# Kernel tuning notes

Measured on AMD Instinct MI355X. Metric: run time of the kernel, lower is better.

Reference implementation:

```python
import jax, jax.numpy as jnp
import numpy as np

B, T, D_MODEL = 1, 2048, 4096
NUM_Q_HEADS, NUM_KV_HEADS, KEY_SIZE = 32, 8, 128
ATTN_MULT = 0.08838834764831845  # 1/sqrt(key_size)
MAX_ATTN_VAL = 30.0


def rotate_half(x):
    x1, x2 = jnp.split(x, 2, axis=-1)
    return jnp.concatenate((-x2, x1), axis=-1)


def apply_rope(x):
    # x: [b, t, h, d]; offset = 0, positions = arange(t)
    b, t, h, d = x.shape
    exponents = jnp.arange(0, d, 2, dtype=jnp.float32)
    inv_freq = 1.0 / (10000.0 ** (exponents / d))            # [d/2]
    pos = jnp.arange(t, dtype=jnp.float32)                   # [t]
    phase = pos[:, None] * inv_freq[None, :]                 # [t, d/2]
    phase = jnp.tile(phase, (1, 2))[None, :, None, :]        # [1, t, 1, d] (tiled, not interleaved)
    return (x * jnp.cos(phase) + rotate_half(x) * jnp.sin(phase)).astype(x.dtype)


def setup_inputs() -> dict:
    key = jax.random.key(0)
    ks = jax.random.split(key, 8)
    query = jax.random.normal(ks[0], (B, T, D_MODEL), dtype=jnp.float32)
    kk = jax.random.normal(ks[1], (B, T, D_MODEL), dtype=jnp.float32)
    vv = jax.random.normal(ks[2], (B, T, D_MODEL), dtype=jnp.float32)
    mask = jnp.tril(jnp.ones((T, T), dtype=bool))[None, None, :, :]  # causal [1,1,T,T]
    s = 0.02
    Wq = jax.random.normal(ks[3], (D_MODEL, NUM_Q_HEADS * KEY_SIZE), dtype=jnp.float32) * s
    Wk = jax.random.normal(ks[4], (D_MODEL, NUM_KV_HEADS * KEY_SIZE), dtype=jnp.float32) * s
    Wv = jax.random.normal(ks[5], (D_MODEL, NUM_KV_HEADS * KEY_SIZE), dtype=jnp.float32) * s
    Wo = jax.random.normal(ks[6], (NUM_Q_HEADS * KEY_SIZE, D_MODEL), dtype=jnp.float32) * s
    return {"query": query, "key": kk, "value": vv, "mask": mask,
            "Wq": Wq, "Wk": Wk, "Wv": Wv, "Wo": Wo}


def reference(query, key, value, mask, Wq, Wk, Wv, Wo):
    b, t, _ = query.shape
    d = KEY_SIZE
    h, kv_h = NUM_Q_HEADS, NUM_KV_HEADS
    g = h // kv_h
    # projections (no bias)
    q = (query @ Wq).reshape(b, t, h, d)
    k = (key @ Wk).reshape(b, t, kv_h, d)
    v = (value @ Wv).reshape(b, t, kv_h, d)
    # RoPE on q and k
    q = apply_rope(q)
    k = apply_rope(k)
    # GQA grouping: [b, t, kv_h, g, d]
    q = q.reshape(b, t, kv_h, g, d)
    logits = jnp.einsum('btkgd,bTkd->bkgtT', q, k).astype(jnp.float32)
    logits = logits * ATTN_MULT
    logits = MAX_ATTN_VAL * jnp.tanh(logits / MAX_ATTN_VAL)  # soft-capping
    m = mask[:, :, None, :, :]  # [b,1,1,t,T]
    logits = jnp.where(m, logits, -1e30)
    weights = jax.nn.softmax(logits, axis=-1).astype(query.dtype)
    attn = jnp.einsum('bkgtT,bTkd->btkgd', weights, v)
    attn = attn.reshape(b, t, h * d)
    return attn @ Wo
```

## Files before the change

kernel.cpp:

```cpp
#include <hip/hip_runtime.h>
#include <hip/hip_bf16.h>
#include <stdint.h>
#include <stddef.h>

#define T_SEQ 2048
#define DM    4096
#define NQH   32
#define NKVH  8
#define HD    128
#define ATTN_MULT 0.08838834764831845f

typedef __attribute__((ext_vector_type(8))) short bf16x8;
typedef __attribute__((ext_vector_type(4))) float f32x4;
typedef __attribute__((ext_vector_type(4))) unsigned int u32x4;

__device__ __forceinline__ unsigned short f2b(float f) {
  unsigned u = __builtin_bit_cast(unsigned, f);
  u = u + 0x7FFFu + ((u >> 16) & 1u);
  return (unsigned short)(u >> 16);
}
__device__ __forceinline__ float b2f(unsigned short h) {
  unsigned u = ((unsigned)h) << 16;
  return __builtin_bit_cast(float, u);
}
__device__ __forceinline__ unsigned cvt_pk_bf16(float lo, float hi) {
  unsigned r;
  asm("v_cvt_pk_bf16_f32 %0, %1, %2" : "=v"(r) : "v"(lo), "v"(hi));
  return r;
}

typedef const __attribute__((address_space(1))) void* gptr1_t;
typedef __attribute__((address_space(3))) void* lptr3_t;
__device__ __forceinline__ void gl_lds16(const void* g, void* l) {
  __builtin_amdgcn_global_load_lds((gptr1_t)g, (lptr3_t)l, 16, 0, 0);
}

#define MFMA16(a, b, c) __builtin_amdgcn_mfma_f32_16x16x32_bf16((a), (b), (c), 0, 0, 0)

__global__ __launch_bounds__(256) void transpose_cast4_kernel(
    const float* __restrict__ Wq, const float* __restrict__ Wk,
    const float* __restrict__ Wv, const float* __restrict__ Wo,
    unsigned short* __restrict__ WqT, unsigned short* __restrict__ WkT,
    unsigned short* __restrict__ WvT, unsigned short* __restrict__ WoT) {
  __shared__ float tile[64][65];
  int y = blockIdx.y;
  const float* W;
  unsigned short* WT;
  int N, n0;
  if (y < 64)      { W = Wq; WT = WqT; N = 4096; n0 = y * 64; }
  else if (y < 80) { W = Wk; WT = WkT; N = 1024; n0 = (y - 64) * 64; }
  else if (y < 96) { W = Wv; WT = WvT; N = 1024; n0 = (y - 80) * 64; }
  else             { W = Wo; WT = WoT; N = 4096; n0 = (y - 96) * 64; }
  const int K = 4096;
  int k0 = blockIdx.x * 64;
  int t = threadIdx.x;
  int rr = t >> 4;
  int cc = t & 15;
#pragma unroll
  for (int c = 0; c < 4; ++c) {
    int row = c * 16 + rr;
    float4 v = *(const float4*)&W[(size_t)(k0 + row) * N + n0 + cc * 4];
    tile[row][cc * 4 + 0] = v.x;
    tile[row][cc * 4 + 1] = v.y;
    tile[row][cc * 4 + 2] = v.z;
    tile[row][cc * 4 + 3] = v.w;
  }
  __syncthreads();
  int orow = t >> 2;
  int kb = (t & 3) * 16;
  u32x4 o1, o2;
#pragma unroll
  for (int u = 0; u < 4; ++u) {
    o1[u] = (unsigned)f2b(tile[kb + 2 * u][orow]) |
            ((unsigned)f2b(tile[kb + 2 * u + 1][orow]) << 16);
    o2[u] = (unsigned)f2b(tile[kb + 8 + 2 * u][orow]) |
            ((unsigned)f2b(tile[kb + 9 + 2 * u][orow]) << 16);
  }
  unsigned short* dst = &WT[(size_t)(n0 + orow) * K + k0 + kb];
  *(u32x4*)dst = o1;
  *(u32x4*)(dst + 8) = o2;
}

__global__ __launch_bounds__(256) void cast3_kernel(
    const float* __restrict__ a0, const float* __restrict__ a1, const float* __restrict__ a2,
    unsigned short* __restrict__ b0, unsigned short* __restrict__ b1, unsigned short* __restrict__ b2) {
  const float* in = blockIdx.z == 0 ? a0 : (blockIdx.z == 1 ? a1 : a2);
  unsigned short* out = blockIdx.z == 0 ? b0 : (blockIdx.z == 1 ? b1 : b2);
  size_t idx = ((size_t)blockIdx.x * 256 + threadIdx.x) * 8;
  float4 x = *(const float4*)(in + idx);
  float4 y = *(const float4*)(in + idx + 4);
  u32x4 v;
  v[0] = (unsigned)f2b(x.x) | ((unsigned)f2b(x.y) << 16);
  v[1] = (unsigned)f2b(x.z) | ((unsigned)f2b(x.w) << 16);
  v[2] = (unsigned)f2b(y.x) | ((unsigned)f2b(y.y) << 16);
  v[3] = (unsigned)f2b(y.z) | ((unsigned)f2b(y.w) << 16);
  *(u32x4*)(out + idx) = v;
}

template <bool F32OUT>
__device__ __forceinline__ void gemm256_body(
    unsigned short* lds,
    const unsigned short* __restrict__ A, const unsigned short* __restrict__ BT,
    void* __restrict__ C, int N, int Klen, int Kstride, int m0, int n0) {
  int t = threadIdx.x;
  int w = t >> 6, l = t & 63;
  int wm = w >> 2, wn = w & 3;
  int lr = l & 15, lh = l >> 4;

  f32x4 acc[8][4] = {};

  int scb = (((l & 7) ^ (l >> 3)) & 7) << 4;
  const int NT = Klen >> 6;
  int rswz = (lr & 7) << 4;
  int cb0 = (lh * 16) ^ rswz;
  int cb1 = (64 + lh * 16) ^ rswz;

  auto stageT = [&](const unsigned short* X, int base, int tt, int c, int ldsoff) {
#pragma unroll
    for (int h = 0; h < 2; ++h) {
      int grow = base + h * 128 + w * 8 + (l >> 3);
      const char* s1 = (const char*)X + ((size_t)grow * Kstride + tt * 64) * 2 + scb;
      gl_lds16(s1, (char*)lds + c * 65536 + ldsoff + h * 16384 + w * 1024);
      const char* s2 = (const char*)X + ((size_t)(grow + 64) * Kstride + tt * 64) * 2 + scb;
      gl_lds16(s2, (char*)lds + c * 65536 + ldsoff + h * 16384 + 8192 + w * 1024);
    }
  };

  stageT(A, m0, 0, 0, 0);
  stageT(BT, n0, 0, 0, 32768);
  asm volatile("s_waitcnt vmcnt(0)" ::: "memory");
  __builtin_amdgcn_s_barrier();

  for (int tt = 0; tt < NT; ++tt) {
    const char* Ab = (const char*)lds + (tt & 1) * 65536;
    const char* Bb = Ab + 32768;
    if (tt + 1 < NT) {
      int nb = (tt + 1) & 1;
      stageT(A, m0, tt + 1, nb, 0);
      stageT(BT, n0, tt + 1, nb, 32768);
    }
    int arow = wm * 128 + lr;
    int brow = wn * 64 + lr;
#pragma unroll
    for (int ks = 0; ks < 2; ++ks) {
      int cb = ks ? cb1 : cb0;
      bf16x8 av[8], bv[4];
#pragma unroll
      for (int i = 0; i < 8; ++i)
        av[i] = *(const bf16x8*)(Ab + (arow + i * 16) * 128 + cb);
#pragma unroll
      for (int j = 0; j < 4; ++j)
        bv[j] = *(const bf16x8*)(Bb + (brow + j * 16) * 128 + cb);
#pragma unroll
      for (int i = 0; i < 8; ++i)
#pragma unroll
        for (int j = 0; j < 4; ++j)
          acc[i][j] = MFMA16(av[i], bv[j], acc[i][j]);
    }
    asm volatile("s_waitcnt vmcnt(0)" ::: "memory");
    __builtin_amdgcn_s_barrier();
  }

#pragma unroll
  for (int i = 0; i < 8; ++i) {
#pragma unroll
    for (int j = 0; j < 4; ++j) {
#pragma unroll
      for (int r = 0; r < 4; ++r) {
        int row = m0 + wm * 128 + i * 16 + lh * 4 + r;
        int col = n0 + wn * 64 + j * 16 + lr;
        if constexpr (F32OUT)
          ((float*)C)[(size_t)row * N + col] = acc[i][j][r];
        else
          ((unsigned short*)C)[(size_t)row * N + col] = f2b(acc[i][j][r]);
      }
    }
  }
}

__global__ __launch_bounds__(512, 1) void qkv256_kernel(
    const unsigned short* __restrict__ qb, const unsigned short* __restrict__ WqT, unsigned short* __restrict__ Qp,
    const unsigned short* __restrict__ kb, const unsigned short* __restrict__ WkT, unsigned short* __restrict__ Kp,
    const unsigned short* __restrict__ vb, const unsigned short* __restrict__ WvT, unsigned short* __restrict__ Vp) {
  __shared__ unsigned short lds[2 * 32768];
  int flat = blockIdx.x;
  const unsigned short *A, *BT;
  unsigned short* C;
  int N, m0, n0;
  if (flat < 128) {
    A = qb; BT = WqT; C = Qp; N = NQH * HD;
    m0 = (flat >> 4) * 256;
    n0 = (flat & 15) * 256;
  } else {
    int lf = flat - 128;
    int sel = lf >> 5;
    int local = lf & 31;
    A = sel ? vb : kb;
    BT = sel ? WvT : WkT;
    C = sel ? Vp : Kp;
    N = NKVH * HD;
    m0 = (local >> 2) * 256;
    n0 = (local & 3) * 256;
  }
  gemm256_body<false>(lds, A, BT, C, N, DM, DM, m0, n0);
}

__global__ __launch_bounds__(512, 1) void oproj256_kernel(
    const unsigned short* __restrict__ A, const unsigned short* __restrict__ BT,
    float* __restrict__ P0, float* __restrict__ P1) {
  __shared__ unsigned short lds[2 * 32768];
  int flat = blockIdx.x;
  int ksl = flat >> 7;
  int local = flat & 127;
  int m0 = (local >> 4) * 256;
  int n0 = (local & 15) * 256;
  gemm256_body<true>(lds, A + ksl * 2048, BT + ksl * 2048,
                     ksl ? P1 : P0, DM, 2048, DM, m0, n0);
}

__global__ __launch_bounds__(256) void reduce_add_kernel(
    const float* __restrict__ P0, const float* __restrict__ P1, float* __restrict__ out) {
  size_t idx = ((size_t)blockIdx.x * 256 + threadIdx.x) * 4;
  float4 a = *(const float4*)(P0 + idx);
  float4 b = *(const float4*)(P1 + idx);
  float4 r;
  r.x = a.x + b.x; r.y = a.y + b.y; r.z = a.z + b.z; r.w = a.w + b.w;
  *(float4*)(out + idx) = r;
}

__global__ __launch_bounds__(256) void rope2_kernel(unsigned short* __restrict__ X,
                                                    int nheads, float scale) {
  int idx = blockIdx.x * 256 + threadIdx.x;
  int i = idx & 63;
  int tpos = idx >> 6;
  float invf = exp2f(-(float)i * (13.287712379549449f / 64.0f));
  float phase = (float)tpos * invf;
  float s, c;
  sincosf(phase, &s, &c);
  unsigned short* row = X + (size_t)tpos * ((size_t)nheads * HD) + i;
  for (int h = 0; h < nheads; ++h) {
    float x1 = b2f(row[0]);
    float x2 = b2f(row[64]);
    row[0] = f2b((x1 * c - x2 * s) * scale);
    row[64] = f2b((x2 * c + x1 * s) * scale);
    row += HD;
  }
}

__global__ __launch_bounds__(256) void vtrans_kernel(
    const unsigned short* __restrict__ V, unsigned short* __restrict__ VT) {
  __shared__ unsigned short tile[64][72];
  int t0 = blockIdx.x * 64;
  int dh0 = blockIdx.y * 64;
  int tid = threadIdx.x;
  int r = tid >> 3;
  int c = (tid & 7) * 8;
#pragma unroll
  for (int p = 0; p < 2; ++p) {
    int row = p * 32 + r;
    bf16x8 v = *(const bf16x8*)&V[(size_t)(t0 + row) * (NKVH * HD) + dh0 + c];
    *(bf16x8*)&tile[row][c] = v;
  }
  __syncthreads();
#pragma unroll
  for (int p = 0; p < 2; ++p) {
    int dr = p * 32 + r;
    u32x4 o;
#pragma unroll
    for (int u = 0; u < 4; ++u) {
      unsigned short lo = tile[c + 2 * u][dr];
      unsigned short hi = tile[c + 2 * u + 1][dr];
      o[u] = (unsigned)lo | ((unsigned)hi << 16);
    }
    *(u32x4*)&VT[(size_t)(dh0 + dr) * T_SEQ + t0 + c] = o;
  }
}

template <bool DIAG>
__device__ __forceinline__ void softmax_frag(const f32x4 s[4], float& lsum, bf16x8 pf[2],
                                             int lr, int lh, int wq) {
  constexpr float C2f = (float)(-60.0 * 1.4426950408889634);
  float pv[4][4];
#pragma unroll
  for (int ct = 0; ct < 4; ++ct) {
#pragma unroll
    for (int r = 0; r < 4; ++r) {
      float u = exp2f(s[ct][r]);
      float p = exp2f(C2f * __builtin_amdgcn_rcpf(u + 1.0f));
      if constexpr (DIAG) {
        int kg = ct * 16 + lh * 4 + r;
        int qg = wq * 16 + lr;
        if (kg > qg) p = 0.0f;
      }
      pv[ct][r] = p;
    }
    lsum += (pv[ct][0] + pv[ct][1]) + (pv[ct][2] + pv[ct][3]);
  }
  unsigned pk[4][2];
#pragma unroll
  for (int ct = 0; ct < 4; ++ct) {
    pk[ct][0] = cvt_pk_bf16(pv[ct][0], pv[ct][1]);
    pk[ct][1] = cvt_pk_bf16(pv[ct][2], pv[ct][3]);
  }
  int s0 = ((lh & 1) << 5) + lr;
  int s1 = s0 + 16;
  bool hi = (lh >= 2);
#pragma unroll
  for (int ks = 0; ks < 2; ++ks) {
    unsigned a0 = (unsigned)__shfl((int)pk[2 * ks][0], s0, 64);
    unsigned a1 = (unsigned)__shfl((int)pk[2 * ks][1], s0, 64);
    unsigned a2 = (unsigned)__shfl((int)pk[2 * ks][0], s1, 64);
    unsigned a3 = (unsigned)__shfl((int)pk[2 * ks][1], s1, 64);
    unsigned b0 = (unsigned)__shfl((int)pk[2 * ks + 1][0], s0, 64);
    unsigned b1 = (unsigned)__shfl((int)pk[2 * ks + 1][1], s0, 64);
    unsigned b2 = (unsigned)__shfl((int)pk[2 * ks + 1][0], s1, 64);
    unsigned b3 = (unsigned)__shfl((int)pk[2 * ks + 1][1], s1, 64);
    u32x4 f;
    f[0] = hi ? b0 : a0;
    f[1] = hi ? b1 : a1;
    f[2] = hi ? b2 : a2;
    f[3] = hi ? b3 : a3;
    pf[ks] = __builtin_bit_cast(bf16x8, f);
  }
}

template <bool WITHA, bool DIAGA, bool DIAGB>
__device__ __forceinline__ void attn_tile(
    const char* KsCur, const char* VsCur,
    const bf16x8 qfA[4], const bf16x8 qfB[4],
    f32x4 oaccA[8], f32x4 oaccB[8],
    float& lsumA, float& lsumB,
    int lr, int lh, int wq) {
  f32x4 sB[4], sA[4];
#pragma unroll
  for (int ct = 0; ct < 4; ++ct) {
    f32x4 zB = {};
    f32x4 zA = {};
#pragma unroll
    for (int kk = 0; kk < 4; ++kk) {
      int row = ct * 16 + lr;
      int cb = (kk * 32 + lh * 8) * 2;
      bf16x8 kf = *(const bf16x8*)(KsCur + row * 256 + (cb ^ ((row & 7) << 4)));
      zB = MFMA16(kf, qfB[kk], zB);
      if constexpr (WITHA) zA = MFMA16(kf, qfA[kk], zA);
    }
    sB[ct] = zB;
    if constexpr (WITHA) sA[ct] = zA;
  }
  bf16x8 pfB[2], pfA[2];
  softmax_frag<DIAGB>(sB, lsumB, pfB, lr, lh, wq);
  if constexpr (WITHA) softmax_frag<DIAGA>(sA, lsumA, pfA, lr, lh, wq);
#pragma unroll
  for (int ks = 0; ks < 2; ++ks) {
    int pcb = (ks * 32 + lh * 8) * 2;
#pragma unroll
    for (int dt = 0; dt < 8; ++dt) {
      int vrow = dt * 16 + lr;
      bf16x8 vf = *(const bf16x8*)(VsCur + ((vrow * 128 + pcb) ^ ((vrow & 7) << 4)));
      oaccB[dt] = MFMA16(pfB[ks], vf, oaccB[dt]);
      if constexpr (WITHA) oaccA[dt] = MFMA16(pfA[ks], vf, oaccA[dt]);
    }
  }
}

__global__ __launch_bounds__(512, 2) void attn_kernel(
    const unsigned short* __restrict__ Q,
    const unsigned short* __restrict__ Kx,
    const unsigned short* __restrict__ VT,
    unsigned short* __restrict__ O) {
  __shared__ unsigned short Ks[2][64 * 128];
  __shared__ unsigned short Vs[2][128 * 64];

  int bx = blockIdx.x;
  int by = blockIdx.y;
  int qtA = bx, qtB = 31 - bx;
  int t = threadIdx.x;
  int w = t >> 6, l = t & 63;
  int wq = w & 3;
  int hh = by * 2 + (w >> 2);
  int kvh = by >> 1;
  int lr = l & 15, lh = l >> 4;

  bf16x8 qfA[4], qfB[4];
  {
    const unsigned short* qpA = Q + (size_t)(qtA * 64 + wq * 16 + lr) * (NQH * HD) + hh * HD + lh * 8;
    const unsigned short* qpB = Q + (size_t)(qtB * 64 + wq * 16 + lr) * (NQH * HD) + hh * HD + lh * 8;
#pragma unroll
    for (int kk = 0; kk < 4; ++kk) {
      qfA[kk] = *(const bf16x8*)(qpA + kk * 32);
      qfB[kk] = *(const bf16x8*)(qpB + kk * 32);
    }
  }

  f32x4 oaccA[8] = {}, oaccB[8] = {};
  float lsumA = 0.f, lsumB = 0.f;

  const char* KgB = (const char*)Kx + (size_t)kvh * HD * 2;
  const char* VgB = (const char*)VT + (size_t)kvh * HD * T_SEQ * 2;

  auto stage = [&](int kt, int b) {
#pragma unroll
    for (int c = 0; c < 2; ++c) {
      int chunk = w * 2 + c;
      int p = chunk * 1024 + l * 16;
      {
        int row = p >> 8;
        int cb = p & 255;
        int cbl = cb ^ ((row & 7) << 4);
        gl_lds16(KgB + (size_t)(kt * 64 + row) * (NKVH * HD * 2) + cbl,
                 (char*)Ks[b] + chunk * 1024);
      }
      {
        int row = p >> 7;
        int cb = p & 127;
        int cbl = cb ^ ((row & 7) << 4);
        gl_lds16(VgB + (size_t)row * (T_SEQ * 2) + (size_t)kt * 128 + cbl,
                 (char*)Vs[b] + chunk * 1024);
      }
    }
  };

  stage(0, 0);
  __syncthreads();

  int cur = 0;
  for (int kt = 0; kt <= qtB; ++kt) {
    if (kt < qtB) stage(kt + 1, cur ^ 1);
    const char* Kc = (const char*)Ks[cur];
    const char* Vc = (const char*)Vs[cur];
    if (kt < qtA)
      attn_tile<true, false, false>(Kc, Vc, qfA, qfB, oaccA, oaccB, lsumA, lsumB, lr, lh, wq);
    else if (kt == qtA)
      attn_tile<true, true, false>(Kc, Vc, qfA, qfB, oaccA, oaccB, lsumA, lsumB, lr, lh, wq);
    else if (kt < qtB)
      attn_tile<false, false, false>(Kc, Vc, qfA, qfB, oaccA, oaccB, lsumA, lsumB, lr, lh, wq);
    else
      attn_tile<false, false, true>(Kc, Vc, qfA, qfB, oaccA, oaccB, lsumA, lsumB, lr, lh, wq);
    __syncthreads();
    cur ^= 1;
  }

  lsumB += __shfl_xor(lsumB, 16, 64);
  lsumB += __shfl_xor(lsumB, 32, 64);
  lsumA += __shfl_xor(lsumA, 16, 64);
  lsumA += __shfl_xor(lsumA, 32, 64);

#pragma unroll
  for (int i = 0; i < 4; ++i) {
    int srcl = (l & 48) | (lh * 4 + i);
    float invB = 1.0f / __shfl(lsumB, srcl, 64);
    float invA = 1.0f / __shfl(lsumA, srcl, 64);
    int qgB = qtB * 64 + wq * 16 + lh * 4 + i;
    int qgA = qtA * 64 + wq * 16 + lh * 4 + i;
#pragma unroll
    for (int dt = 0; dt < 8; ++dt) {
      O[(size_t)qgB * (NQH * HD) + hh * HD + dt * 16 + lr] = f2b(oaccB[dt][i] * invB);
      O[(size_t)qgA * (NQH * HD) + hh * HD + dt * 16 + lr] = f2b(oaccA[dt][i] * invA);
    }
  }
}

extern "C" void kernel_launch(void* const* d_in, const int* in_sizes, int n_in,
                              void* d_out, int out_size, void* d_ws, size_t ws_size,
                              hipStream_t stream) {
  const float* query = (const float*)d_in[0];
  const float* key = (const float*)d_in[1];
  const float* value = (const float*)d_in[2];
  const float* Wq = (const float*)d_in[4];
  const float* Wk = (const float*)d_in[5];
  const float* Wv = (const float*)d_in[6];
  const float* Wo = (const float*)d_in[7];
  float* out = (float*)d_out;

  char* ws = (char*)d_ws;
  constexpr size_t OFF_WQT = 0;
  constexpr size_t OFF_WOT = 33554432;
  constexpr size_t OFF_WKT = 67108864;
  constexpr size_t OFF_WVT = 75497472;
  constexpr size_t OFF_QB = 83886080;
  constexpr size_t OFF_KB = 100663296;
  constexpr size_t OFF_VB = 117440512;
  constexpr size_t OFF_QP = 134217728;
  constexpr size_t OFF_KP = 150994944;
  constexpr size_t OFF_VP = 155189248;
  constexpr size_t OFF_VT = 159383552;
  constexpr size_t OFF_AT = 163577856;
  constexpr size_t WS_NEED = 180355072;
  if (ws_size < WS_NEED) return;

  unsigned short* WqT = (unsigned short*)(ws + OFF_WQT);
  unsigned short* WoT = (unsigned short*)(ws + OFF_WOT);
  unsigned short* WkT = (unsigned short*)(ws + OFF_WKT);
  unsigned short* WvT = (unsigned short*)(ws + OFF_WVT);
  unsigned short* qb = (unsigned short*)(ws + OFF_QB);
  unsigned short* kb = (unsigned short*)(ws + OFF_KB);
  unsigned short* vb = (unsigned short*)(ws + OFF_VB);
  unsigned short* Qp = (unsigned short*)(ws + OFF_QP);
  unsigned short* Kp = (unsigned short*)(ws + OFF_KP);
  unsigned short* Vp = (unsigned short*)(ws + OFF_VP);
  unsigned short* VTb = (unsigned short*)(ws + OFF_VT);
  unsigned short* attnb = (unsigned short*)(ws + OFF_AT);
  float* P0 = (float*)(ws + OFF_QB);
  float* P1 = (float*)(ws + OFF_VB);

  transpose_cast4_kernel<<<dim3(64, 160), 256, 0, stream>>>(
      Wq, Wk, Wv, Wo, WqT, WkT, WvT, WoT);
  cast3_kernel<<<dim3(4096, 1, 3), 256, 0, stream>>>(query, key, value, qb, kb, vb);
  qkv256_kernel<<<dim3(192), 512, 0, stream>>>(qb, WqT, Qp, kb, WkT, Kp, vb, WvT, Vp);
  constexpr float C1 = (float)(0.08838834764831845 * 1.4426950408889634 / 15.0);
  rope2_kernel<<<dim3(T_SEQ * 64 / 256), 256, 0, stream>>>(Qp, NQH, C1);
  rope2_kernel<<<dim3(T_SEQ * 64 / 256), 256, 0, stream>>>(Kp, NKVH, 1.0f);
  vtrans_kernel<<<dim3(T_SEQ / 64, NKVH * HD / 64), 256, 0, stream>>>(Vp, VTb);
  attn_kernel<<<dim3(16, 16), 512, 0, stream>>>(Qp, Kp, VTb, attnb);
  oproj256_kernel<<<dim3(256), 512, 0, stream>>>(attnb, WoT, P0, P1);
  reduce_add_kernel<<<dim3(T_SEQ * DM / (256 * 4)), 256, 0, stream>>>(P0, P1, out);
}
```

Baseline: 362.6 us.

## Replace double-buffered GEMM K loop with 4-slot, 32-wide K pipeline

```diff
diff --git a/kernel.cpp b/kernel.cpp
--- a/kernel.cpp
+++ b/kernel.cpp
@@ -109,57 +109,57 @@
 
   f32x4 acc[8][4] = {};
 
-  int scb = (((l & 7) ^ (l >> 3)) & 7) << 4;
-  const int NT = Klen >> 6;
-  int rswz = (lr & 7) << 4;
-  int cb0 = (lh * 16) ^ rswz;
-  int cb1 = (64 + lh * 16) ^ rswz;
-
-  auto stageT = [&](const unsigned short* X, int base, int tt, int c, int ldsoff) {
-#pragma unroll
-    for (int h = 0; h < 2; ++h) {
-      int grow = base + h * 128 + w * 8 + (l >> 3);
-      const char* s1 = (const char*)X + ((size_t)grow * Kstride + tt * 64) * 2 + scb;
-      gl_lds16(s1, (char*)lds + c * 65536 + ldsoff + h * 16384 + w * 1024);
-      const char* s2 = (const char*)X + ((size_t)(grow + 64) * Kstride + tt * 64) * 2 + scb;
-      gl_lds16(s2, (char*)lds + c * 65536 + ldsoff + h * 16384 + 8192 + w * 1024);
+  const int NH = Klen >> 5;
+  int srow = w * 32 + (l >> 2);
+  int gcb = (((l & 3) ^ ((l >> 2) & 3) ^ (l >> 4)) << 4);
+  int rcb = ((lh ^ (lr & 3) ^ ((lr >> 2) & 3)) << 4);
+  int arow = wm * 128 + lr;
+  int brow = wn * 64 + lr;
+  const size_t ksb = (size_t)Kstride * 2;
+
+  auto stage = [&](int h) {
+    int slot = h & 3;
+    char* Asl = (char*)lds + slot * 32768;
+    char* Bsl = Asl + 16384;
+    const char* Ag = (const char*)A + (size_t)h * 64 + gcb;
+    const char* Bg = (const char*)BT + (size_t)h * 64 + gcb;
+#pragma unroll
+    for (int ld = 0; ld < 2; ++ld) {
+      int r = srow + ld * 16;
+      gl_lds16(Ag + (size_t)(m0 + r) * ksb, Asl + w * 2048 + ld * 1024);
+      gl_lds16(Bg + (size_t)(n0 + r) * ksb, Bsl + w * 2048 + ld * 1024);
     }
   };
 
-  stageT(A, m0, 0, 0, 0);
-  stageT(BT, n0, 0, 0, 32768);
-  asm volatile("s_waitcnt vmcnt(0)" ::: "memory");
-  __builtin_amdgcn_s_barrier();
-
-  for (int tt = 0; tt < NT; ++tt) {
-    const char* Ab = (const char*)lds + (tt & 1) * 65536;
-    const char* Bb = Ab + 32768;
-    if (tt + 1 < NT) {
-      int nb = (tt + 1) & 1;
-      stageT(A, m0, tt + 1, nb, 0);
-      stageT(BT, n0, tt + 1, nb, 32768);
-    }
-    int arow = wm * 128 + lr;
-    int brow = wn * 64 + lr;
-#pragma unroll
-    for (int ks = 0; ks < 2; ++ks) {
-      int cb = ks ? cb1 : cb0;
-      bf16x8 av[8], bv[4];
-#pragma unroll
-      for (int i = 0; i < 8; ++i)
-        av[i] = *(const bf16x8*)(Ab + (arow + i * 16) * 128 + cb);
+  auto phase = [&](int h, int wcnt) {
+    if (wcnt == 8)      asm volatile("s_waitcnt vmcnt(8)" ::: "memory");
+    else if (wcnt == 4) asm volatile("s_waitcnt vmcnt(4)" ::: "memory");
+    else                asm volatile("s_waitcnt vmcnt(0)" ::: "memory");
+    __builtin_amdgcn_s_barrier();
+    int slot = h & 3;
+    const char* Asl = (const char*)lds + slot * 32768;
+    const char* Bsl = Asl + 16384;
+    bf16x8 av[8], bv[4];
+#pragma unroll
+    for (int i = 0; i < 8; ++i)
+      av[i] = *(const bf16x8*)(Asl + (arow + i * 16) * 64 + rcb);
+#pragma unroll
+    for (int j = 0; j < 4; ++j)
+      bv[j] = *(const bf16x8*)(Bsl + (brow + j * 16) * 64 + rcb);
+    if (h + 3 < NH) stage(h + 3);
+    __builtin_amdgcn_s_setprio(1);
+#pragma unroll
+    for (int i = 0; i < 8; ++i)
 #pragma unroll
       for (int j = 0; j < 4; ++j)
-        bv[j] = *(const bf16x8*)(Bb + (brow + j * 16) * 128 + cb);
-#pragma unroll
-      for (int i = 0; i < 8; ++i)
-#pragma unroll
-        for (int j = 0; j < 4; ++j)
-          acc[i][j] = MFMA16(av[i], bv[j], acc[i][j]);
-    }
-    asm volatile("s_waitcnt vmcnt(0)" ::: "memory");
-    __builtin_amdgcn_s_barrier();
-  }
+        acc[i][j] = MFMA16(av[i], bv[j], acc[i][j]);
+    __builtin_amdgcn_s_setprio(0);
+  };
+
+  stage(0); stage(1); stage(2);
+  for (int h = 0; h < NH - 2; ++h) phase(h, 8);
+  phase(NH - 2, 4);
+  phase(NH - 1, 0);
 
 #pragma unroll
   for (int i = 0; i < 8; ++i) {
@@ -182,7 +182,7 @@
     const unsigned short* __restrict__ qb, const unsigned short* __restrict__ WqT, unsigned short* __restrict__ Qp,
     const unsigned short* __restrict__ kb, const unsigned short* __restrict__ WkT, unsigned short* __restrict__ Kp,
     const unsigned short* __restrict__ vb, const unsigned short* __restrict__ WvT, unsigned short* __restrict__ Vp) {
-  __shared__ unsigned short lds[2 * 32768];
+  __shared__ unsigned short lds[4 * 16384];
   int flat = blockIdx.x;
   const unsigned short *A, *BT;
   unsigned short* C;
@@ -208,7 +208,7 @@
 __global__ __launch_bounds__(512, 1) void oproj256_kernel(
     const unsigned short* __restrict__ A, const unsigned short* __restrict__ BT,
     float* __restrict__ P0, float* __restrict__ P1) {
-  __shared__ unsigned short lds[2 * 32768];
+  __shared__ unsigned short lds[4 * 16384];
   int flat = blockIdx.x;
   int ksl = flat >> 7;
   int local = flat & 127;
```

Result: slower. 375.3 us (+3.5%).
